# Kernel optimization log

Measured on AMD Instinct MI355X. Metric: run time of the kernel, lower is better.

Reference implementation:

```python
import jax, jax.numpy as jnp
import numpy as np

COMMITMENT_WEIGHT = 0.25


def _vq_layer(residual, codebook):
    """One euclidean VQ layer: nearest-codeword lookup + straight-through.
    residual: [B,T,D], codebook: [K,D].
    Returns (q_st [B,T,D], idx [B,T], commit_loss scalar).
    """
    B, T, D = residual.shape
    flat = residual.reshape(-1, D)  # [N,D]
    d2 = (jnp.sum(flat * flat, axis=-1, keepdims=True)
          - 2.0 * flat @ codebook.T
          + jnp.sum(codebook * codebook, axis=-1))  # [N,K]
    idx = jnp.argmin(d2, axis=-1)                   # [N]
    q = codebook[idx].reshape(B, T, D)
    # straight-through estimator (as in vector_quantize_pytorch)
    q_st = residual + jax.lax.stop_gradient(q - residual)
    commit_loss = COMMITMENT_WEIGHT * jnp.mean(
        (jax.lax.stop_gradient(q) - residual) ** 2)
    return q_st, idx.reshape(B, T), commit_loss


def setup_inputs() -> dict:
    key = jax.random.key(0)
    ks = jax.random.split(key, 9)
    D = 768
    sizes = [2, 4, 8, 16, 32, 64, 128, 256]
    inp = {"x": jax.random.normal(ks[0], (32, 2048, D), dtype=jnp.float32)}
    for i, K in enumerate(sizes):
        inp[f"cb{i}"] = jax.random.normal(ks[i + 1], (K, D), dtype=jnp.float32)
    return inp


def reference(x, cb0, cb1, cb2, cb3, cb4, cb5, cb6, cb7):
    codebooks = [cb0, cb1, cb2, cb3, cb4, cb5, cb6, cb7]
    residual = x
    quantized = jnp.zeros_like(x)
    all_indices = []
    total_commit_loss = jnp.float32(0.0)
    for cb in codebooks:  # fixed 8 structurally-distinct layers
        q, idx, commit = _vq_layer(residual, cb)
        quantized = quantized + q
        residual = residual - q
        all_indices.append(idx)
        total_commit_loss = total_commit_loss + commit
    all_indices = jnp.stack(all_indices, axis=-1)  # [B,T,num_layers]
    return quantized, all_indices, total_commit_loss
```

## Files before the change

### kernel.cpp

```cpp
#include <hip/hip_runtime.h>
#include <stdint.h>

#define NTOK 65536
#define DIM  768
#define NCB  512
#define NC   510
#define TAU  0.75f

typedef _Float16 f16x8 __attribute__((ext_vector_type(8)));
typedef float f32x4 __attribute__((ext_vector_type(4)));

#define WS_C32   0u
#define WS_CHI   1572864u
#define WS_CNORM 3145728u
#define WS_G     3147776u
#define WS_IDX   4196352u
#define WS_PART  6293504u
#define WS_PART2 6359040u
#define WS_S     8388608u
#define S_BYTES  67108864u

__device__ __forceinline__ void gl_lds16(const void* g, void* l){
  __builtin_amdgcn_global_load_lds(
      (const __attribute__((address_space(1))) unsigned int*)g,
      (__attribute__((address_space(3))) unsigned int*)l,
      16, 0, 0);
}

__global__ void k_prep(const float* __restrict__ cb0, const float* __restrict__ cb1,
                       const float* __restrict__ cb2, const float* __restrict__ cb3,
                       const float* __restrict__ cb4, const float* __restrict__ cb5,
                       const float* __restrict__ cb6, const float* __restrict__ cb7,
                       char* __restrict__ ws){
  const int r = blockIdx.x, t = threadIdx.x;
  const float* srcs[8] = {cb0,cb1,cb2,cb3,cb4,cb5,cb6,cb7};
  const int off[8] = {0,2,6,14,30,62,126,254};
  const int KK[8]  = {2,4,8,16,32,64,128,256};
  const float* src = nullptr;
#pragma unroll
  for (int l=0;l<8;l++)
    if (r >= off[l] && r < off[l]+KK[l]) src = srcs[l] + (size_t)(r - off[l]) * DIM;
  float* C32 = (float*)(ws + WS_C32);
  _Float16* Chi = (_Float16*)(ws + WS_CHI);
  double ss = 0.0;
#pragma unroll
  for (int i=0;i<3;i++){
    const int e = t + i*256;
    const float v = src ? src[e] : 0.f;
    C32[(size_t)r*DIM + e] = v;
    Chi[(size_t)r*DIM + e] = (_Float16)v;
    ss += (double)v * (double)v;
  }
  __shared__ double red[256];
  red[t] = ss; __syncthreads();
  for (int sdown=128; sdown>0; sdown>>=1){
    if (t < sdown) red[t] += red[t+sdown];
    __syncthreads();
  }
  if (t == 0){
    float* cnp = (float*)(ws + WS_CNORM);
    cnp[r] = (r < NC) ? (float)red[0] : 1e30f;
  }
}

__global__ void k_gram(char* __restrict__ ws){
  const int i = blockIdx.x, t = threadIdx.x;
  const float* __restrict__ C32 = (const float*)(ws + WS_C32);
  __shared__ float row[DIM];
  for (int e=t; e<DIM; e+=256) row[e] = C32[(size_t)i*DIM + e];
  __syncthreads();
  float* __restrict__ G = (float*)(ws + WS_G);
  for (int j=t; j<NCB; j+=256){
    const float4* cj = (const float4*)(C32 + (size_t)j*DIM);
    double d = 0.0;
    for (int k=0; k<DIM/4; k++){
      const float4 b = cj[k];
      d += (double)row[4*k]*(double)b.x + (double)row[4*k+1]*(double)b.y
         + (double)row[4*k+2]*(double)b.z + (double)row[4*k+3]*(double)b.w;
    }
    G[(size_t)i*NCB + j] = (float)d;
  }
}

__global__ __launch_bounds__(256, 3) void k_gemm(const float* __restrict__ x,
                                                 const char* __restrict__ ws,
                                                 _Float16* __restrict__ S,
                                                 float* __restrict__ part2){
  __shared__ __align__(16) char smem[49152];
  const int t = threadIdx.x, lane = t & 63, w = t >> 6;
  const int wm = w >> 1, wn = w & 1;
  const int bid = blockIdx.x;
  const int xcd = bid & 7, jj = bid >> 3;
  const int mt = xcd*64 + (jj >> 2), nt = jj & 3;
  const _Float16* __restrict__ Chi = (const _Float16*)(ws + WS_CHI);

  f32x4 acc[4][4];
#pragma unroll
  for (int i=0;i<4;i++)
#pragma unroll
    for (int j=0;j<4;j++) acc[i][j] = {0.f,0.f,0.f,0.f};

  float xs = 0.f;

  for (int kt=0; kt<12; kt++){
#pragma unroll
    for (int i8=0;i8<8;i8++){
      const int r0 = w*32 + i8*4;
      const int row = r0 + (lane>>4);
      const int g = lane & 15;
      const int sg = g ^ (((row&7)<<1) | ((row>>3)&1));
      const size_t go = (size_t)(mt*128 + row)*DIM + (size_t)kt*64 + sg*4;
      gl_lds16(x + go, smem + r0*256);
    }
#pragma unroll
    for (int c4=0;c4<4;c4++){
      const int r0 = w*32 + c4*8;
      const int rloc = r0 + (lane>>3);
      const int jsrc = (lane&7) ^ (rloc&7);
      const size_t go = (size_t)(nt*128 + rloc)*DIM + (size_t)kt*64 + jsrc*8;
      gl_lds16(Chi + go, smem + 32768 + r0*128);
    }
    __syncthreads();
    if ((kt & 3) == nt){
#pragma unroll
      for (int g=0; g<8; g++){
        const f32x4 v = *(const f32x4*)(smem + t*128 + g*16);
        xs += v[0]*v[0] + v[1]*v[1] + v[2]*v[2] + v[3]*v[3];
      }
    }
#pragma unroll
    for (int kk=0; kk<2; kk++){
      f16x8 fa[4], fb[4];
#pragma unroll
      for (int mf=0;mf<4;mf++){
        const int m = wm*64 + mf*16 + (lane&15);
        const int maskm = ((m&7)<<1) | ((m>>3)&1);
        const int ch = kk*4 + (lane>>4);
        const int g0 = (2*ch) ^ maskm;
        const f32x4 lo = *(const f32x4*)(smem + m*256 + g0*16);
        const f32x4 hi = *(const f32x4*)(smem + m*256 + (g0^1)*16);
        f16x8 r;
        r[0]=(_Float16)lo[0]; r[1]=(_Float16)lo[1]; r[2]=(_Float16)lo[2]; r[3]=(_Float16)lo[3];
        r[4]=(_Float16)hi[0]; r[5]=(_Float16)hi[1]; r[6]=(_Float16)hi[2]; r[7]=(_Float16)hi[3];
        fa[mf] = r;
      }
#pragma unroll
      for (int nf=0;nf<4;nf++){
        const int c = wn*64 + nf*16 + (lane&15);
        const uint bb = (uint)(32768 + c*128 + ((((kk<<2)+(lane>>4)) ^ (c&7))*16));
        fb[nf] = *(const f16x8*)(smem + bb);
      }
#pragma unroll
      for (int mf=0;mf<4;mf++)
#pragma unroll
        for (int nf=0;nf<4;nf++)
          acc[mf][nf] = __builtin_amdgcn_mfma_f32_16x16x32_f16(fa[mf], fb[nf], acc[mf][nf], 0,0,0);
    }
    __syncthreads();
  }

#pragma unroll
  for (int d=32; d>0; d>>=1) xs += __shfl_down(xs, d);
  if (lane == 0) ((float*)smem)[w] = xs;
  __syncthreads();
  if (t == 0) part2[bid] = ((float*)smem)[0] + ((float*)smem)[1]
                         + ((float*)smem)[2] + ((float*)smem)[3];

#pragma unroll
  for (int mf=0;mf<4;mf++)
#pragma unroll
    for (int nf=0;nf<4;nf++){
      const f32x4 v = acc[mf][nf];
      const int col  = nt*128 + wn*64 + nf*16 + (lane&15);
      const int row0 = mt*128 + wm*64 + mf*16 + ((lane>>4)<<2);
#pragma unroll
      for (int e=0;e<4;e++)
        S[(size_t)(row0+e)*NCB + col] = (_Float16)v[e];
    }
}

template<int FUSED>
__global__ __launch_bounds__(512, 4) void k_chain(const float* __restrict__ x,
                                                  const _Float16* __restrict__ S,
                                                  char* __restrict__ ws,
                                                  float* __restrict__ out,
                                                  float* __restrict__ part){
  const int t = threadIdx.x, lane = t & 63, w = t >> 6;
  const size_t tok = (size_t)blockIdx.x*8 + w;
  const float* __restrict__ cn  = (const float*)(ws + WS_CNORM);
  const float* __restrict__ G   = (const float*)(ws + WS_G);
  const float* __restrict__ C32 = (const float*)(ws + WS_C32);

  float sv[8], s0[8], cnv[8];
  {
    const uint* sp = (const uint*)(S + tok*NCB);
#pragma unroll
    for (int j=0;j<4;j++){
      union { uint u; _Float16 h[2]; } cv;
      cv.u = sp[j*64 + lane];
      sv[2*j]   = (float)cv.h[0];
      sv[2*j+1] = (float)cv.h[1];
      const float2 c2 = *(const float2*)(cn + j*128 + lane*2);
      cnv[2*j] = c2.x; cnv[2*j+1] = c2.y;
    }
  }
#pragma unroll
  for (int k=0;k<8;k++) s0[k] = sv[k];

  int mcs[8];
  float tot = 0.f;

#pragma unroll
  for (int l=0; l<8; ++l){
    const int cs = (2<<l) - 2;
    const int ce = cs + (2<<l);
    float bv = 3e38f; int bc = 511;
#pragma unroll
    for (int j=0;j<4;j++){
      const int c0 = j*128 + lane*2;
      const float sA = (c0   >= cs && c0   < ce) ? (cnv[2*j]   - 2.f*sv[2*j])   : 3e38f;
      const float sB = (c0+1 >= cs && c0+1 < ce) ? (cnv[2*j+1] - 2.f*sv[2*j+1]) : 3e38f;
      if (sA < bv){ bv = sA; bc = c0; }
      if (sB < bv){ bv = sB; bc = c0+1; }
    }
    uint u = __float_as_uint(bv);
    u ^= (u & 0x80000000u) ? 0xFFFFFFFFu : 0x80000000u;
    uint key = (u & 0xFFFFFE00u) | ((uint)bc & 511u);
#pragma unroll
    for (int d=1; d<64; d<<=1){
      const uint ok = (uint)__shfl_xor((int)key, d);
      key = (ok < key) ? ok : key;
    }
    const int mc0 = (int)(key & 511u);
    const uint vq = key & 0xFFFFFE00u;
    const uint sb = (vq & 0x80000000u) ? (vq ^ 0x80000000u) : ~vq;
    const float bv_est = __uint_as_float(sb);

    int bm = 0;
#pragma unroll
    for (int j=0;j<4;j++){
      const int c0 = j*128 + lane*2;
      const float sA = (c0   >= cs && c0   < ce) ? (cnv[2*j]   - 2.f*sv[2*j])   : 3e38f;
      const float sB = (c0+1 >= cs && c0+1 < ce) ? (cnv[2*j+1] - 2.f*sv[2*j+1]) : 3e38f;
      if (sA <= bv_est + TAU) bm |= 1 << (2*j);
      if (sB <= bv_est + TAU) bm |= 1 << (2*j+1);
    }
    const unsigned long long lmask = __ballot(bm != 0);
    const int b0 = __ffsll((long long)lmask) - 1;
    const int bm0 = __shfl(bm, b0);
    const bool multi = (__popcll(lmask) > 1) || ((bm0 & (bm0-1)) != 0);

    int mc = mc0;
    float ssel = bv_est;
    if (multi){
      float xv[12];
      {
        const float4* xp = (const float4*)(x + tok*DIM + lane*12);
#pragma unroll
        for (int q=0;q<3;q++){
          const float4 v = xp[q];
          xv[q*4]=v.x; xv[q*4+1]=v.y; xv[q*4+2]=v.z; xv[q*4+3]=v.w;
        }
      }
      double bve = 1e300; int bce = 0x7fffffff;
      unsigned long long Lm = lmask;
      while (Lm){
        const int b = __ffsll((long long)Lm) - 1; Lm &= Lm - 1;
        const int mbits = __shfl(bm, b);
#pragma unroll
        for (int k=0;k<8;k++){
          if (mbits & (1<<k)){
            const int c = (k>>1)*128 + b*2 + (k&1);
            const float dkv = __shfl(s0[k] - sv[k], b);
            const float* __restrict__ crow = C32 + (size_t)c*DIM + lane*12;
            double dd = 0.0;
#pragma unroll
            for (int q=0;q<3;q++){
              const float4 v = *(const float4*)(crow + q*4);
              dd += (double)xv[q*4]*v.x + (double)xv[q*4+1]*v.y
                  + (double)xv[q*4+2]*v.z + (double)xv[q*4+3]*v.w;
            }
#pragma unroll
            for (int d=1; d<64; d<<=1) dd += __shfl_xor(dd, d);
            const double se = (double)cn[c] - 2.0*(dd - (double)dkv);
            if (se < bve || (se == bve && c < bce)){ bve = se; bce = c; }
          }
        }
      }
      mc = bce;
      ssel = (float)bve;
    }
    mcs[l] = mc;
    if (FUSED) tot += (float)(8 - l) * ssel;
    if (l < 7){
      const float* __restrict__ gr = G + (size_t)mc*NCB;
#pragma unroll
      for (int j=0;j<4;j++){
        const float2 g2 = *(const float2*)(gr + j*128 + lane*2);
        sv[2*j] -= g2.x; sv[2*j+1] -= g2.y;
      }
    }
  }

  if (FUSED){
    float q[12];
#pragma unroll
    for (int i=0;i<12;i++) q[i] = 0.f;
#pragma unroll
    for (int l=0;l<8;l++){
      const float* __restrict__ cw = C32 + (size_t)mcs[l]*DIM + lane*12;
#pragma unroll
      for (int qq=0;qq<3;qq++){
        const float4 v = *(const float4*)(cw + qq*4);
        q[qq*4]+=v.x; q[qq*4+1]+=v.y; q[qq*4+2]+=v.z; q[qq*4+3]+=v.w;
      }
    }
    float* op = out + tok*DIM + lane*12;
#pragma unroll
    for (int qq=0;qq<3;qq++){
      float4 v; v.x=q[qq*4]; v.y=q[qq*4+1]; v.z=q[qq*4+2]; v.w=q[qq*4+3];
      *(float4*)(op + qq*4) = v;
    }
    if (lane == 0){
      float4 i0, i1;
      i0.x=(float)(mcs[0]-0);   i0.y=(float)(mcs[1]-2);   i0.z=(float)(mcs[2]-6);   i0.w=(float)(mcs[3]-14);
      i1.x=(float)(mcs[4]-30);  i1.y=(float)(mcs[5]-62);  i1.z=(float)(mcs[6]-126); i1.w=(float)(mcs[7]-254);
      *(float4*)(out + (size_t)NTOK*DIM + tok*8)     = i0;
      *(float4*)(out + (size_t)NTOK*DIM + tok*8 + 4) = i1;
    }
    __shared__ float bs[8];
    if (lane == 0) bs[w] = tot;
    __syncthreads();
    if (t == 0){
      float s2 = 0.f;
#pragma unroll
      for (int j=0;j<8;j++) s2 += bs[j];
      part[blockIdx.x] = s2;
    }
  } else {
    if (lane == 0){
      int* idxw = (int*)(ws + WS_IDX);
      const int offs[8] = {0,2,6,14,30,62,126,254};
#pragma unroll
      for (int l=0;l<8;l++) idxw[tok*8 + l] = mcs[l] - offs[l];
    }
  }
}

__global__ __launch_bounds__(512) void k_fin(const float* __restrict__ x,
                                             char* __restrict__ ws,
                                             float* __restrict__ out,
                                             float* __restrict__ part){
  const int t = threadIdx.x, lane = t & 63, w = t >> 6;
  const size_t tok = (size_t)blockIdx.x * 8 + w;
  const int off[8] = {0,2,6,14,30,62,126,254};
  const int* __restrict__ idxw = (const int*)(ws + WS_IDX);
  const float* __restrict__ C32 = (const float*)(ws + WS_C32);
  int loc[8];
#pragma unroll
  for (int l=0;l<8;l++) loc[l] = idxw[tok*8 + l];
  if (lane < 8) out[(size_t)NTOK*DIM + tok*8 + lane] = (float)idxw[tok*8 + lane];

  const float4* __restrict__ xr = (const float4*)(x + tok*DIM);
  float4* __restrict__ qr = (float4*)(out + tok*DIM);
  const float4* crow[8];
#pragma unroll
  for (int l=0;l<8;l++) crow[l] = (const float4*)(C32 + (size_t)(loc[l] + off[l])*DIM);
  float ssq = 0.f;
#pragma unroll
  for (int i=0;i<3;i++){
    const int e4 = i*64 + lane;
    const float4 xv = xr[e4];
    float rx = xv.x, ry = xv.y, rz = xv.z, rw = xv.w;
    float qx = 0.f, qy = 0.f, qz = 0.f, qw = 0.f;
#pragma unroll
    for (int l=0;l<8;l++){
      const float4 cv = crow[l][e4];
      rx -= cv.x; ry -= cv.y; rz -= cv.z; rw -= cv.w;
      qx += cv.x; qy += cv.y; qz += cv.z; qw += cv.w;
      ssq += rx*rx + ry*ry + rz*rz + rw*rw;
    }
    float4 q; q.x = qx; q.y = qy; q.z = qz; q.w = qw;
    qr[e4] = q;
  }
#pragma unroll
  for (int d=32; d>0; d>>=1) ssq += __shfl_down(ssq, d);
  __shared__ float bsum[8];
  if (lane == 0) bsum[w] = ssq;
  __syncthreads();
  if (t == 0){
    float s2 = 0.f;
#pragma unroll
    for (int j=0;j<8;j++) s2 += bsum[j];
    part[blockIdx.x] = s2;
  }
}

__global__ void k_loss(const float* __restrict__ part, int n,
                       const float* __restrict__ part2, int n2,
                       float* __restrict__ out){
  const int t = threadIdx.x;
  double s = 0.0;
  for (int i=t; i<n; i+=256) s += (double)part[i];
  double sx = 0.0;
  for (int i=t; i<n2; i+=256) sx += (double)part2[i];
  __shared__ double red[256];
  red[t] = s + 8.0*sx; __syncthreads();
  for (int d=128; d>0; d>>=1){
    if (t < d) red[t] += red[t+d];
    __syncthreads();
  }
  if (t == 0)
    out[(size_t)NTOK*DIM + (size_t)NTOK*8] =
      (float)(0.25 * red[0] / (double)((size_t)NTOK * DIM));
}

extern "C" void kernel_launch(void* const* d_in, const int* in_sizes, int n_in,
                              void* d_out, int out_size, void* d_ws, size_t ws_size,
                              hipStream_t stream){
  const float* x = (const float*)d_in[0];
  char* ws = (char*)d_ws;
  float* out = (float*)d_out;
  float* part  = (float*)(ws + WS_PART);
  float* part2 = (float*)(ws + WS_PART2);
  const bool fused = ws_size >= (size_t)WS_S + (size_t)S_BYTES;
  _Float16* Sp = fused ? (_Float16*)(ws + WS_S) : (_Float16*)out;

  k_prep<<<512, 256, 0, stream>>>((const float*)d_in[1], (const float*)d_in[2],
                                  (const float*)d_in[3], (const float*)d_in[4],
                                  (const float*)d_in[5], (const float*)d_in[6],
                                  (const float*)d_in[7], (const float*)d_in[8], ws);
  k_gram<<<512, 256, 0, stream>>>(ws);
  k_gemm<<<2048, 256, 0, stream>>>(x, ws, Sp, part2);
  if (fused){
    k_chain<1><<<8192, 512, 0, stream>>>(x, Sp, ws, out, part);
    k_loss<<<1, 256, 0, stream>>>(part, 8192, part2, 2048, out);
  } else {
    k_chain<0><<<8192, 512, 0, stream>>>(x, Sp, ws, out, part);
    k_fin<<<8192, 512, 0, stream>>>(x, ws, out, part);
    k_loss<<<1, 256, 0, stream>>>(part, 8192, (const float*)nullptr, 0, out);
  }
}
```

Before: 362.3 us.

## Load GEMM A operand directly to registers, triple-buffer B, fold norms into scores

```diff
diff --git a/kernel.cpp b/kernel.cpp
--- a/kernel.cpp
+++ b/kernel.cpp
@@ -5,7 +5,7 @@
 #define DIM  768
 #define NCB  512
 #define NC   510
-#define TAU  0.75f
+#define TAU  1.0f
 
 typedef _Float16 f16x8 __attribute__((ext_vector_type(8)));
 typedef float f32x4 __attribute__((ext_vector_type(4)));
@@ -78,14 +78,14 @@
       d += (double)row[4*k]*(double)b.x + (double)row[4*k+1]*(double)b.y
          + (double)row[4*k+2]*(double)b.z + (double)row[4*k+3]*(double)b.w;
     }
-    G[(size_t)i*NCB + j] = (float)d;
-  }
-}
-
-__global__ __launch_bounds__(256, 3) void k_gemm(const float* __restrict__ x,
-                                                 const char* __restrict__ ws,
-                                                 _Float16* __restrict__ S,
-                                                 float* __restrict__ part2){
+    G[(size_t)i*NCB + j] = (float)(2.0*d);
+  }
+}
+
+__global__ __launch_bounds__(256) void k_gemm(const float* __restrict__ x,
+                                              const char* __restrict__ ws,
+                                              _Float16* __restrict__ Sq,
+                                              float* __restrict__ part2){
   __shared__ __align__(16) char smem[49152];
   const int t = threadIdx.x, lane = t & 63, w = t >> 6;
   const int wm = w >> 1, wn = w & 1;
@@ -93,6 +93,7 @@
   const int xcd = bid & 7, jj = bid >> 3;
   const int mt = xcd*64 + (jj >> 2), nt = jj & 3;
   const _Float16* __restrict__ Chi = (const _Float16*)(ws + WS_CHI);
+  const float* __restrict__ cn = (const float*)(ws + WS_CNORM);
 
   f32x4 acc[4][4];
 #pragma unroll
@@ -100,71 +101,96 @@
 #pragma unroll
     for (int j=0;j<4;j++) acc[i][j] = {0.f,0.f,0.f,0.f};
 
+  const float* xb0 = x + (size_t)(mt*128 + wm*64 + 0*16 + (lane&15))*DIM + (lane>>4)*8;
+  const float* xb1 = xb0 + 16*DIM;
+  const float* xb2 = xb0 + 32*DIM;
+  const float* xb3 = xb0 + 48*DIM;
+
+  float4 va[16];
   float xs = 0.f;
 
+#define LOAD_A(kt_)                                                          \
+  {                                                                          \
+    const float* p0 = xb0 + (kt_)*64; const float* p1 = xb1 + (kt_)*64;      \
+    const float* p2 = xb2 + (kt_)*64; const float* p3 = xb3 + (kt_)*64;      \
+    va[0]=*(const float4*)(p0);    va[1]=*(const float4*)(p0+4);             \
+    va[2]=*(const float4*)(p0+32); va[3]=*(const float4*)(p0+36);            \
+    va[4]=*(const float4*)(p1);    va[5]=*(const float4*)(p1+4);             \
+    va[6]=*(const float4*)(p1+32); va[7]=*(const float4*)(p1+36);            \
+    va[8]=*(const float4*)(p2);    va[9]=*(const float4*)(p2+4);             \
+    va[10]=*(const float4*)(p2+32);va[11]=*(const float4*)(p2+36);           \
+    va[12]=*(const float4*)(p3);   va[13]=*(const float4*)(p3+4);            \
+    va[14]=*(const float4*)(p3+32);va[15]=*(const float4*)(p3+36);           \
+  }
+
+#define STAGE_B(kt_, base_)                                                  \
+  {                                                                          \
+    _Pragma("unroll")                                                        \
+    for (int c4=0;c4<4;c4++){                                                \
+      const int r0 = w*32 + c4*8;                                            \
+      const int rloc = r0 + (lane>>3);                                       \
+      const int jsrc = (lane&7) ^ (rloc&7);                                  \
+      const size_t go = (size_t)(nt*128 + rloc)*DIM + (size_t)(kt_)*64 + jsrc*8; \
+      gl_lds16(Chi + go, smem + (base_) + r0*128);                           \
+    }                                                                        \
+  }
+
+#define COMPUTE(bbase_)                                                      \
+  {                                                                          \
+    _Pragma("unroll")                                                        \
+    for (int kk=0; kk<2; kk++){                                              \
+      f16x8 fa[4], fb[4];                                                    \
+      _Pragma("unroll")                                                      \
+      for (int mf=0;mf<4;mf++){                                              \
+        const float4 lo = va[mf*4 + kk*2];                                   \
+        const float4 hi = va[mf*4 + kk*2 + 1];                               \
+        f16x8 r;                                                             \
+        r[0]=(_Float16)lo.x; r[1]=(_Float16)lo.y; r[2]=(_Float16)lo.z; r[3]=(_Float16)lo.w; \
+        r[4]=(_Float16)hi.x; r[5]=(_Float16)hi.y; r[6]=(_Float16)hi.z; r[7]=(_Float16)hi.w; \
+        fa[mf] = r;                                                          \
+      }                                                                      \
+      _Pragma("unroll")                                                      \
+      for (int nf=0;nf<4;nf++){                                              \
+        const int c = wn*64 + nf*16 + (lane&15);                             \
+        const uint bb = (bbase_) + (uint)(c*128 + ((((kk<<2)+(lane>>4)) ^ (c&7))*16)); \
+        fb[nf] = *(const f16x8*)(smem + bb);                                 \
+      }                                                                      \
+      _Pragma("unroll")                                                      \
+      for (int mf=0;mf<4;mf++)                                               \
+        _Pragma("unroll")                                                    \
+        for (int nf=0;nf<4;nf++)                                             \
+          acc[mf][nf] = __builtin_amdgcn_mfma_f32_16x16x32_f16(fa[mf], fb[nf], acc[mf][nf], 0,0,0); \
+    }                                                                        \
+  }
+
+  STAGE_B(0, 0u);
+  LOAD_A(0);
+
+#pragma unroll
   for (int kt=0; kt<12; kt++){
-#pragma unroll
-    for (int i8=0;i8<8;i8++){
-      const int r0 = w*32 + i8*4;
-      const int row = r0 + (lane>>4);
-      const int g = lane & 15;
-      const int sg = g ^ (((row&7)<<1) | ((row>>3)&1));
-      const size_t go = (size_t)(mt*128 + row)*DIM + (size_t)kt*64 + sg*4;
-      gl_lds16(x + go, smem + r0*256);
-    }
-#pragma unroll
-    for (int c4=0;c4<4;c4++){
-      const int r0 = w*32 + c4*8;
-      const int rloc = r0 + (lane>>3);
-      const int jsrc = (lane&7) ^ (rloc&7);
-      const size_t go = (size_t)(nt*128 + rloc)*DIM + (size_t)kt*64 + jsrc*8;
-      gl_lds16(Chi + go, smem + 32768 + r0*128);
-    }
+    if (kt+1 < 12) STAGE_B(kt+1, (uint)(16384*((kt+1)%3)));
+    if (kt < 11) { asm volatile("s_waitcnt vmcnt(20)" ::: "memory"); }
+    else         { asm volatile("s_waitcnt vmcnt(0)"  ::: "memory"); }
+    __builtin_amdgcn_s_barrier();
+    __builtin_amdgcn_sched_barrier(0);
+    if (nt == 0 && wn == 0){
+#pragma unroll
+      for (int q=0;q<16;q++)
+        xs += va[q].x*va[q].x + va[q].y*va[q].y + va[q].z*va[q].z + va[q].w*va[q].w;
+    }
+    COMPUTE((uint)(16384*(kt%3)));
+    if (kt+1 < 12) LOAD_A(kt+1);
+  }
+
+  __syncthreads();
+  if (nt == 0){
+    float* sb = (float*)smem;
+#pragma unroll
+    for (int d=32; d>0; d>>=1) xs += __shfl_down(xs, d);
+    if (wn == 0 && lane == 0) sb[wm] = xs;
     __syncthreads();
-    if ((kt & 3) == nt){
-#pragma unroll
-      for (int g=0; g<8; g++){
-        const f32x4 v = *(const f32x4*)(smem + t*128 + g*16);
-        xs += v[0]*v[0] + v[1]*v[1] + v[2]*v[2] + v[3]*v[3];
-      }
-    }
-#pragma unroll
-    for (int kk=0; kk<2; kk++){
-      f16x8 fa[4], fb[4];
-#pragma unroll
-      for (int mf=0;mf<4;mf++){
-        const int m = wm*64 + mf*16 + (lane&15);
-        const int maskm = ((m&7)<<1) | ((m>>3)&1);
-        const int ch = kk*4 + (lane>>4);
-        const int g0 = (2*ch) ^ maskm;
-        const f32x4 lo = *(const f32x4*)(smem + m*256 + g0*16);
-        const f32x4 hi = *(const f32x4*)(smem + m*256 + (g0^1)*16);
-        f16x8 r;
-        r[0]=(_Float16)lo[0]; r[1]=(_Float16)lo[1]; r[2]=(_Float16)lo[2]; r[3]=(_Float16)lo[3];
-        r[4]=(_Float16)hi[0]; r[5]=(_Float16)hi[1]; r[6]=(_Float16)hi[2]; r[7]=(_Float16)hi[3];
-        fa[mf] = r;
-      }
-#pragma unroll
-      for (int nf=0;nf<4;nf++){
-        const int c = wn*64 + nf*16 + (lane&15);
-        const uint bb = (uint)(32768 + c*128 + ((((kk<<2)+(lane>>4)) ^ (c&7))*16));
-        fb[nf] = *(const f16x8*)(smem + bb);
-      }
-#pragma unroll
-      for (int mf=0;mf<4;mf++)
-#pragma unroll
-        for (int nf=0;nf<4;nf++)
-          acc[mf][nf] = __builtin_amdgcn_mfma_f32_16x16x32_f16(fa[mf], fb[nf], acc[mf][nf], 0,0,0);
-    }
-    __syncthreads();
-  }
-
-#pragma unroll
-  for (int d=32; d>0; d>>=1) xs += __shfl_down(xs, d);
-  if (lane == 0) ((float*)smem)[w] = xs;
-  __syncthreads();
-  if (t == 0) part2[bid] = ((float*)smem)[0] + ((float*)smem)[1]
-                         + ((float*)smem)[2] + ((float*)smem)[3];
+    if (t == 0) part2[mt] = sb[0] + sb[1];
+  }
 
 #pragma unroll
   for (int mf=0;mf<4;mf++)
@@ -173,10 +199,14 @@
       const f32x4 v = acc[mf][nf];
       const int col  = nt*128 + wn*64 + nf*16 + (lane&15);
       const int row0 = mt*128 + wm*64 + mf*16 + ((lane>>4)<<2);
+      const float cnc = cn[col];
 #pragma unroll
       for (int e=0;e<4;e++)
-        S[(size_t)(row0+e)*NCB + col] = (_Float16)v[e];
-    }
+        Sq[(size_t)(row0+e)*NCB + col] = (_Float16)(cnc - 2.f*v[e] - 768.f);
+    }
+#undef LOAD_A
+#undef STAGE_B
+#undef COMPUTE
 }
 
 template<int FUSED>
@@ -188,10 +218,10 @@
   const int t = threadIdx.x, lane = t & 63, w = t >> 6;
   const size_t tok = (size_t)blockIdx.x*8 + w;
   const float* __restrict__ cn  = (const float*)(ws + WS_CNORM);
-  const float* __restrict__ G   = (const float*)(ws + WS_G);
+  const float* __restrict__ G2  = (const float*)(ws + WS_G);
   const float* __restrict__ C32 = (const float*)(ws + WS_C32);
 
-  float sv[8], s0[8], cnv[8];
+  float sv[8], s0[8];
   {
     const uint* sp = (const uint*)(S + tok*NCB);
 #pragma unroll
@@ -200,8 +230,6 @@
       cv.u = sp[j*64 + lane];
       sv[2*j]   = (float)cv.h[0];
       sv[2*j+1] = (float)cv.h[1];
-      const float2 c2 = *(const float2*)(cn + j*128 + lane*2);
-      cnv[2*j] = c2.x; cnv[2*j+1] = c2.y;
     }
   }
 #pragma unroll
@@ -218,8 +246,8 @@
 #pragma unroll
     for (int j=0;j<4;j++){
       const int c0 = j*128 + lane*2;
-      const float sA = (c0   >= cs && c0   < ce) ? (cnv[2*j]   - 2.f*sv[2*j])   : 3e38f;
-      const float sB = (c0+1 >= cs && c0+1 < ce) ? (cnv[2*j+1] - 2.f*sv[2*j+1]) : 3e38f;
+      const float sA = (c0   >= cs && c0   < ce) ? sv[2*j]   : 3e38f;
+      const float sB = (c0+1 >= cs && c0+1 < ce) ? sv[2*j+1] : 3e38f;
       if (sA < bv){ bv = sA; bc = c0; }
       if (sB < bv){ bv = sB; bc = c0+1; }
     }
@@ -235,15 +263,14 @@
     const uint vq = key & 0xFFFFFE00u;
     const uint sb = (vq & 0x80000000u) ? (vq ^ 0x80000000u) : ~vq;
     const float bv_est = __uint_as_float(sb);
+    const float thr = bv_est + TAU;
 
     int bm = 0;
 #pragma unroll
     for (int j=0;j<4;j++){
       const int c0 = j*128 + lane*2;
-      const float sA = (c0   >= cs && c0   < ce) ? (cnv[2*j]   - 2.f*sv[2*j])   : 3e38f;
-      const float sB = (c0+1 >= cs && c0+1 < ce) ? (cnv[2*j+1] - 2.f*sv[2*j+1]) : 3e38f;
-      if (sA <= bv_est + TAU) bm |= 1 << (2*j);
-      if (sB <= bv_est + TAU) bm |= 1 << (2*j+1);
+      if (c0   >= cs && c0   < ce && sv[2*j]   <= thr) bm |= 1 << (2*j);
+      if (c0+1 >= cs && c0+1 < ce && sv[2*j+1] <= thr) bm |= 1 << (2*j+1);
     }
     const unsigned long long lmask = __ballot(bm != 0);
     const int b0 = __ffsll((long long)lmask) - 1;
@@ -251,7 +278,7 @@
     const bool multi = (__popcll(lmask) > 1) || ((bm0 & (bm0-1)) != 0);
 
     int mc = mc0;
-    float ssel = bv_est;
+    float ssel = bv_est + 768.f;
     if (multi){
       float xv[12];
       {
@@ -271,7 +298,7 @@
         for (int k=0;k<8;k++){
           if (mbits & (1<<k)){
             const int c = (k>>1)*128 + b*2 + (k&1);
-            const float dkv = __shfl(s0[k] - sv[k], b);
+            const float dkv = __shfl((sv[k] - s0[k]) * 0.5f, b);
             const float* __restrict__ crow = C32 + (size_t)c*DIM + lane*12;
             double dd = 0.0;
 #pragma unroll
@@ -293,11 +320,11 @@
     mcs[l] = mc;
     if (FUSED) tot += (float)(8 - l) * ssel;
     if (l < 7){
-      const float* __restrict__ gr = G + (size_t)mc*NCB;
+      const float* __restrict__ gr = G2 + (size_t)mc*NCB;
 #pragma unroll
       for (int j=0;j<4;j++){
         const float2 g2 = *(const float2*)(gr + j*128 + lane*2);
-        sv[2*j] -= g2.x; sv[2*j+1] -= g2.y;
+        sv[2*j] += g2.x; sv[2*j+1] += g2.y;
       }
     }
   }
@@ -434,10 +461,10 @@
   k_gemm<<<2048, 256, 0, stream>>>(x, ws, Sp, part2);
   if (fused){
     k_chain<1><<<8192, 512, 0, stream>>>(x, Sp, ws, out, part);
-    k_loss<<<1, 256, 0, stream>>>(part, 8192, part2, 2048, out);
+    k_loss<<<1, 256, 0, stream>>>(part, 8192, part2, 512, out);
   } else {
     k_chain<0><<<8192, 512, 0, stream>>>(x, Sp, ws, out, part);
     k_fin<<<8192, 512, 0, stream>>>(x, ws, out, part);
-    k_loss<<<1, 256, 0, stream>>>(part, 8192, (const float*)nullptr, 0, out);
-  }
-}
+    k_loss<<<1, 256, 0, stream>>>(part, 8192, part2, 512, out);
+  }
+}
```

Result: slower. 476.1 us (+31.4%).
